# Kernel tuning notes

Hardware: AMD Instinct MI355X
Metric: run time of the kernel (lower is better)

Reference implementation:

```python
import jax, jax.numpy as jnp
import numpy as np

N, E, D = 50000, 600000, 128  # nodes, edges, units (== vert_dim, so no W_adapt)


def glorot(key, shape):
    lim = np.sqrt(6.0 / (shape[0] + shape[1]))
    return jax.random.uniform(key, shape, jnp.float32, -lim, lim)


def setup_inputs() -> dict:
    key = jax.random.key(0)
    ks = jax.random.split(key, 8)
    X = jax.random.normal(ks[0], (N, D), jnp.float32)
    ref_a = jax.random.randint(ks[1], (E,), 0, N, jnp.int32)
    ref_b = jax.random.randint(ks[2], (E,), 0, N, jnp.int32)
    # msg_net: two Dense(D) layers, inner_activation=None (linear)
    W1 = glorot(ks[3], (D, D)); b1 = jnp.zeros((D,), jnp.float32)
    W2 = glorot(ks[4], (D, D)); b2 = jnp.zeros((D,), jnp.float32)
    # keras GRUCell (reset_after=True): kernel [D,3D], recurrent_kernel [D,3D], bias [2,3D]
    gru_kernel = glorot(ks[5], (D, 3 * D))
    gru_rkernel = glorot(ks[6], (D, 3 * D))
    gru_bias = jnp.zeros((2, 3 * D), jnp.float32)
    return {"X": X, "ref_a": ref_a, "ref_b": ref_b,
            "W1": W1, "b1": b1, "W2": W2, "b2": b2,
            "gru_kernel": gru_kernel, "gru_rkernel": gru_rkernel, "gru_bias": gru_bias}


def _ggnn(X, ref_a, ref_b, W1, b1, W2, b2, gru_kernel, gru_rkernel, gru_bias):
    # msg_net (depth=2, linear inner activation)
    X_msg = (X @ W1 + b1) @ W2 + b2                       # [N, D]
    # wl1_convolution, undirected: scatter-add both directions
    agg = jnp.zeros_like(X_msg)
    agg = agg.at[ref_b].add(X_msg[ref_a])                 # a -> b
    agg = agg.at[ref_a].add(X_msg[ref_b])                 # b -> a (directed=False)
    # keras GRUCell update: inputs = agg, state = X  (reset_after=True)
    mx = agg @ gru_kernel + gru_bias[0]                   # [N, 3D]
    mh = X @ gru_rkernel + gru_bias[1]                    # [N, 3D]
    xz, xr, xh = jnp.split(mx, 3, axis=-1)
    rz, rr, rh = jnp.split(mh, 3, axis=-1)
    z = jax.nn.sigmoid(xz + rz)
    r = jax.nn.sigmoid(xr + rr)
    hh = jnp.tanh(xh + r * rh)
    return z * X + (1.0 - z) * hh                         # [N, D]


def reference(X, ref_a, ref_b, W1, b1, W2, b2, gru_kernel, gru_rkernel, gru_bias):
    return _ggnn(X, ref_a, ref_b, W1, b1, W2, b2, gru_kernel, gru_rkernel, gru_bias)
```

## Files before the change

kernel.cpp:

```cpp
#include <hip/hip_runtime.h>
#include <cstdint>
#include <cstddef>

typedef __bf16 bf16x8 __attribute__((ext_vector_type(8)));
typedef float  f32x4  __attribute__((ext_vector_type(4)));
typedef short  s16x8  __attribute__((ext_vector_type(8)));

static __device__ __forceinline__ float bf2f(short s) {
    union { unsigned u; float f; } v;
    v.u = ((unsigned)(unsigned short)s) << 16;
    return v.f;
}
static __device__ __forceinline__ short f2bf(float f) {
    unsigned u = __float_as_uint(f);
    u += 0x7fffu + ((u >> 16) & 1u);
    return (short)(u >> 16);
}
static __device__ __forceinline__ float rcp_(float x) {
    return __builtin_amdgcn_rcpf(x);
}
static __device__ __forceinline__ float sigmoid_(float x) {
    return rcp_(1.0f + __expf(-x));
}
static __device__ __forceinline__ float tanh_(float x) {
    float ax = fabsf(x);
    float e  = __expf(-2.0f * ax);
    float t  = (1.0f - e) * rcp_(1.0f + e);
    return copysignf(t, x);
}

#define MFMA(a, b, c) __builtin_amdgcn_mfma_f32_16x16x32_bf16((a), (b), (c), 0, 0, 0)

static __device__ __forceinline__ int lidx8(int r, int ch) {
    return r * 128 + ((ch ^ (r & 15)) << 3);
}
static __device__ __forceinline__ int lidx(int r, int col) {
    return r * 128 + ((((col >> 3) ^ (r & 15)) << 3) | (col & 7));
}

#define BLOCKS1     256
#define STRIPE_CAP  32
#define BUCKET_REG  (BLOCKS1 * STRIPE_CAP)
#define NODE_CAP    96

static __device__ __forceinline__ s16x8 cvt8(const float* p) {
    f32x4 a0 = *(const f32x4*)(p);
    f32x4 a1 = *(const f32x4*)(p + 4);
    s16x8 v;
    v[0] = f2bf(a0[0]); v[1] = f2bf(a0[1]); v[2] = f2bf(a0[2]); v[3] = f2bf(a0[3]);
    v[4] = f2bf(a1[0]); v[5] = f2bf(a1[1]); v[6] = f2bf(a1[2]); v[7] = f2bf(a1[3]);
    return v;
}

__global__ __launch_bounds__(512) void pass1_msg_kernel(
    const int* __restrict__ ra, const int* __restrict__ rb,
    unsigned* __restrict__ bucketed, int* __restrict__ stripeCnt,
    int E, int CPB, int nbk,
    const float* __restrict__ GK, const float* __restrict__ GR,
    short* __restrict__ GKt, short* __restrict__ GRt,
    const float* __restrict__ X,
    const float* __restrict__ W1, const float* __restrict__ b1,
    const float* __restrict__ W2, const float* __restrict__ b2,
    short* __restrict__ msg, int N)
{
    __shared__ short ldsA[64 * 128];
    __shared__ short ldsY[64 * 128];
    __shared__ int cnt[1024];
    const int tid = threadIdx.x;

    if ((int)blockIdx.x < BLOCKS1) {
        for (int b = tid; b < nbk; b += 512) cnt[b] = 0;

        int i = blockIdx.x * 512 + tid;
        if (i < 49152) {
            int k = i / 384, n = i - k * 384;
            GKt[n * 128 + k] = f2bf(GK[i]);
            GRt[n * 128 + k] = f2bf(GR[i]);
        }
        __syncthreads();

        const int blk = blockIdx.x;
        const int e1 = min(E, (blk + 1) * CPB);
        for (int e = blk * CPB + tid; e < e1; e += 512) {
            int a = ra[e], b = rb[e];
            int ka = a >> 6, kb = b >> 6;
            int r1 = atomicAdd(&cnt[ka], 1);
            if (r1 < STRIPE_CAP)
                bucketed[(size_t)ka * BUCKET_REG + blk * STRIPE_CAP + r1] =
                    ((unsigned)(a & 63) << 16) | (unsigned)b;
            int r2 = atomicAdd(&cnt[kb], 1);
            if (r2 < STRIPE_CAP)
                bucketed[(size_t)kb * BUCKET_REG + blk * STRIPE_CAP + r2] =
                    ((unsigned)(b & 63) << 16) | (unsigned)a;
        }
        __syncthreads();
        for (int b = tid; b < nbk; b += 512)
            stripeCnt[(size_t)b * BLOCKS1 + blk] = min(cnt[b], STRIPE_CAP);
        return;
    }

    const int m0   = (blockIdx.x - BLOCKS1) * 64;
    const int lane = tid & 63, wv = tid >> 6;
    const int q = lane >> 4, c = lane & 15;
    const int ncol = wv * 16 + c;

    bf16x8 w1f[4], w2f[4];
#pragma unroll
    for (int ks = 0; ks < 4; ks++) {
        s16x8 v1, v2;
#pragma unroll
        for (int t = 0; t < 8; t++) {
            int k = ks * 32 + q * 8 + t;
            v1[t] = f2bf(W1[(size_t)k * 128 + ncol]);
            v2[t] = f2bf(W2[(size_t)k * 128 + ncol]);
        }
        w1f[ks] = __builtin_bit_cast(bf16x8, v1);
        w2f[ks] = __builtin_bit_cast(bf16x8, v2);
    }

    for (int i = tid; i < 64 * 16; i += 512) {
        int r = i >> 4, ch = i & 15;
        s16x8 v;
        if (m0 + r < N) v = cvt8(X + (size_t)(m0 + r) * 128 + ch * 8);
        else            v = (s16x8)0;
        *(s16x8*)(ldsA + lidx8(r, ch)) = v;
    }
    __syncthreads();

    f32x4 acc[4];
#pragma unroll
    for (int rt = 0; rt < 4; rt++) acc[rt] = (f32x4)0.0f;
#pragma unroll
    for (int ks = 0; ks < 4; ks++) {
        int kc = ks * 4 + q;
#pragma unroll
        for (int rt = 0; rt < 4; rt++) {
            bf16x8 aA = __builtin_bit_cast(bf16x8, *(const s16x8*)(ldsA + lidx8(rt * 16 + c, kc)));
            acc[rt] = MFMA(aA, w1f[ks], acc[rt]);
        }
    }
    float bias1 = b1[ncol];
#pragma unroll
    for (int rt = 0; rt < 4; rt++)
#pragma unroll
        for (int i = 0; i < 4; i++)
            ldsY[lidx(rt * 16 + q * 4 + i, ncol)] = f2bf(acc[rt][i] + bias1);
    __syncthreads();

#pragma unroll
    for (int rt = 0; rt < 4; rt++) acc[rt] = (f32x4)0.0f;
#pragma unroll
    for (int ks = 0; ks < 4; ks++) {
        int kc = ks * 4 + q;
#pragma unroll
        for (int rt = 0; rt < 4; rt++) {
            bf16x8 aY = __builtin_bit_cast(bf16x8, *(const s16x8*)(ldsY + lidx8(rt * 16 + c, kc)));
            acc[rt] = MFMA(aY, w2f[ks], acc[rt]);
        }
    }
    float bias2 = b2[ncol];
#pragma unroll
    for (int rt = 0; rt < 4; rt++)
#pragma unroll
        for (int i = 0; i < 4; i++) {
            int row = m0 + rt * 16 + q * 4 + i;
            if (row < N) msg[(size_t)row * 128 + ncol] = f2bf(acc[rt][i] + bias2);
        }
}

__global__ __launch_bounds__(512) void slab_gather_kernel(
    const unsigned* __restrict__ bucketed, const int* __restrict__ stripeCnt,
    const short* __restrict__ msg, short* __restrict__ aggb, int N)
{
    __shared__ unsigned short slab[64 * NODE_CAP];
    __shared__ int off[64];
    __shared__ int scnt[BLOCKS1];
    const int tid = threadIdx.x;
    const int b   = blockIdx.x;

    if (tid < 64) off[tid] = 0;
    if (tid < BLOCKS1) scnt[tid] = stripeCnt[(size_t)b * BLOCKS1 + tid];
    __syncthreads();

    const unsigned* reg = bucketed + (size_t)b * BUCKET_REG;
    for (int i = tid; i < BUCKET_REG; i += 512) {
        if ((i & (STRIPE_CAP - 1)) < scnt[i >> 5]) {
            unsigned e = reg[i];
            int nl = (int)(e >> 16);
            int p  = (int)(e & 0xffffu);
            int r  = atomicAdd(&off[nl], 1);
            if (r < NODE_CAP)
                slab[nl * NODE_CAP + r] = (unsigned short)p;
        }
    }
    __syncthreads();

    const int lane = tid & 63, wv = tid >> 6;
    const int q  = lane >> 4;
    const int cl = lane & 15;

    for (int k = 0; k < 8; k++) {
        const int nl   = wv * 8 + k;
        const int node = b * 64 + nl;
        float a[8];
#pragma unroll
        for (int t = 0; t < 8; t++) a[t] = 0.0f;
        if (node < N) {
            const int deg = min(off[nl], NODE_CAP);
            const unsigned short* lst = slab + nl * NODE_CAP;
            int i = q;
            for (; i + 12 < deg; i += 16) {
                int j0 = (int)lst[i];
                int j1 = (int)lst[i + 4];
                int j2 = (int)lst[i + 8];
                int j3 = (int)lst[i + 12];
                s16x8 p0 = *(const s16x8*)(msg + (size_t)j0 * 128 + cl * 8);
                s16x8 p1 = *(const s16x8*)(msg + (size_t)j1 * 128 + cl * 8);
                s16x8 p2 = *(const s16x8*)(msg + (size_t)j2 * 128 + cl * 8);
                s16x8 p3 = *(const s16x8*)(msg + (size_t)j3 * 128 + cl * 8);
#pragma unroll
                for (int t = 0; t < 8; t++) a[t] += bf2f(p0[t]);
#pragma unroll
                for (int t = 0; t < 8; t++) a[t] += bf2f(p1[t]);
#pragma unroll
                for (int t = 0; t < 8; t++) a[t] += bf2f(p2[t]);
#pragma unroll
                for (int t = 0; t < 8; t++) a[t] += bf2f(p3[t]);
            }
            for (; i + 4 < deg; i += 8) {
                int j0 = (int)lst[i];
                int j1 = (int)lst[i + 4];
                s16x8 p0 = *(const s16x8*)(msg + (size_t)j0 * 128 + cl * 8);
                s16x8 p1 = *(const s16x8*)(msg + (size_t)j1 * 128 + cl * 8);
#pragma unroll
                for (int t = 0; t < 8; t++) a[t] += bf2f(p0[t]);
#pragma unroll
                for (int t = 0; t < 8; t++) a[t] += bf2f(p1[t]);
            }
            if (i < deg) {
                int j = (int)lst[i];
                s16x8 p = *(const s16x8*)(msg + (size_t)j * 128 + cl * 8);
#pragma unroll
                for (int t = 0; t < 8; t++) a[t] += bf2f(p[t]);
            }
        }
#pragma unroll
        for (int t = 0; t < 8; t++) {
            a[t] += __shfl_xor(a[t], 32);
            a[t] += __shfl_xor(a[t], 16);
        }
        if (q == 0 && b * 64 + nl < N) {
            s16x8 o;
#pragma unroll
            for (int t = 0; t < 8; t++) o[t] = f2bf(a[t]);
            *(s16x8*)(aggb + (size_t)(b * 64 + nl) * 128 + cl * 8) = o;
        }
    }
}

__global__ __launch_bounds__(512) void gru_kernel(
    const short* __restrict__ aggb, const float* __restrict__ X,
    const short* __restrict__ GKt, const short* __restrict__ GRt,
    const float* __restrict__ gbias, float* __restrict__ out, int N)
{
    __shared__ short ldsA[64 * 128];
    __shared__ short ldsX[64 * 128];
    const int tid  = threadIdx.x;
    const int m0   = blockIdx.x * 64;
    const int lane = tid & 63, wv = tid >> 6;
    const int q = lane >> 4, c = lane & 15;
    const int ncol = wv * 16 + c;

    bf16x8 bkz[4], bkr[4], bkh[4], brz[4], brr[4], brh[4];
#pragma unroll
    for (int ks = 0; ks < 4; ks++) {
        int ko = ks * 32 + q * 8;
        bkz[ks] = __builtin_bit_cast(bf16x8, *(const s16x8*)(GKt + (size_t)(ncol)       * 128 + ko));
        bkr[ks] = __builtin_bit_cast(bf16x8, *(const s16x8*)(GKt + (size_t)(128 + ncol) * 128 + ko));
        bkh[ks] = __builtin_bit_cast(bf16x8, *(const s16x8*)(GKt + (size_t)(256 + ncol) * 128 + ko));
        brz[ks] = __builtin_bit_cast(bf16x8, *(const s16x8*)(GRt + (size_t)(ncol)       * 128 + ko));
        brr[ks] = __builtin_bit_cast(bf16x8, *(const s16x8*)(GRt + (size_t)(128 + ncol) * 128 + ko));
        brh[ks] = __builtin_bit_cast(bf16x8, *(const s16x8*)(GRt + (size_t)(256 + ncol) * 128 + ko));
    }
    float bz0 = gbias[ncol],       br0 = gbias[128 + ncol],       bh0 = gbias[256 + ncol];
    float bz1 = gbias[384 + ncol], br1 = gbias[384 + 128 + ncol], bh1 = gbias[384 + 256 + ncol];

    for (int i = tid; i < 64 * 16; i += 512) {
        int r = i >> 4, ch = i & 15;
        s16x8 vx, va;
        if (m0 + r < N) {
            vx = cvt8(X + (size_t)(m0 + r) * 128 + ch * 8);
            va = *(const s16x8*)(aggb + (size_t)(m0 + r) * 128 + ch * 8);
        } else { vx = (s16x8)0; va = (s16x8)0; }
        *(s16x8*)(ldsX + lidx8(r, ch)) = vx;
        *(s16x8*)(ldsA + lidx8(r, ch)) = va;
    }
    __syncthreads();

#pragma clang loop unroll(disable)
    for (int rt = 0; rt < 4; rt++) {
        float xv[4];
#pragma unroll
        for (int i = 0; i < 4; i++) {
            int grow = m0 + rt * 16 + q * 4 + i;
            xv[i] = (grow < N) ? X[(size_t)grow * 128 + ncol] : 0.0f;
        }
        f32x4 axz = (f32x4)0.0f, axr = (f32x4)0.0f, axh = (f32x4)0.0f;
        f32x4 arz = (f32x4)0.0f, arr = (f32x4)0.0f, arh = (f32x4)0.0f;
#pragma unroll
        for (int ks = 0; ks < 4; ks++) {
            int kc = ks * 4 + q;
            bf16x8 aA = __builtin_bit_cast(bf16x8, *(const s16x8*)(ldsA + lidx8(rt * 16 + c, kc)));
            bf16x8 aX = __builtin_bit_cast(bf16x8, *(const s16x8*)(ldsX + lidx8(rt * 16 + c, kc)));
            axz = MFMA(aA, bkz[ks], axz);
            axr = MFMA(aA, bkr[ks], axr);
            axh = MFMA(aA, bkh[ks], axh);
            arz = MFMA(aX, brz[ks], arz);
            arr = MFMA(aX, brr[ks], arr);
            arh = MFMA(aX, brh[ks], arh);
        }
#pragma unroll
        for (int i = 0; i < 4; i++) {
            int grow = m0 + rt * 16 + q * 4 + i;
            if (grow < N) {
                float z  = sigmoid_(axz[i] + bz0 + arz[i] + bz1);
                float r  = sigmoid_(axr[i] + br0 + arr[i] + br1);
                float hh = tanh_(axh[i] + bh0 + r * (arh[i] + bh1));
                out[(size_t)grow * 128 + ncol] = z * xv[i] + (1.0f - z) * hh;
            }
        }
    }
}

extern "C" void kernel_launch(void* const* d_in, const int* in_sizes, int n_in,
                              void* d_out, int out_size, void* d_ws, size_t ws_size,
                              hipStream_t stream)
{
    const float* X  = (const float*)d_in[0];
    const int*   ra = (const int*)d_in[1];
    const int*   rb = (const int*)d_in[2];
    const float* W1 = (const float*)d_in[3];
    const float* b1 = (const float*)d_in[4];
    const float* W2 = (const float*)d_in[5];
    const float* b2 = (const float*)d_in[6];
    const float* GK = (const float*)d_in[7];
    const float* GR = (const float*)d_in[8];
    const float* GB = (const float*)d_in[9];
    const int N = in_sizes[0] / 128;
    const int E = in_sizes[1];
    float* out = (float*)d_out;

    const int nbk = (N + 63) / 64;

    char* ws = (char*)d_ws;
    size_t off = 0;
    short* aggb   = (short*)(ws + off);   off += (size_t)N * 128 * 2;
    short* msg    = (short*)(ws + off);   off += (size_t)N * 128 * 2;
    short* GKt    = (short*)(ws + off);   off += 49152u * 2;
    short* GRt    = (short*)(ws + off);   off += 49152u * 2;
    unsigned* bucketed = (unsigned*)(ws + off);
    off += (size_t)nbk * BUCKET_REG * 4;
    int* stripeCnt = (int*)(ws + off);    off += (size_t)nbk * BLOCKS1 * 4;

    const int CPB = (E + BLOCKS1 - 1) / BLOCKS1;

    pass1_msg_kernel<<<BLOCKS1 + nbk, 512, 0, stream>>>(
        ra, rb, bucketed, stripeCnt, E, CPB, nbk,
        GK, GR, GKt, GRt,
        X, W1, b1, W2, b2, msg, N);

    slab_gather_kernel<<<nbk, 512, 0, stream>>>(bucketed, stripeCnt, msg, aggb, N);

    gru_kernel<<<nbk, 512, 0, stream>>>(aggb, X, GKt, GRt, GB, out, N);
}
```

Measured before the change: 200.9 us.

## Fuse slab gather and GRU update into one tail kernel via LDS

Merges the neighbor-aggregation gather kernel with the GRU kernel so the aggregated bf16 rows are written straight into shared memory and consumed by the MFMA GRU step in the same block. This removes the global aggb round trip (write plus read of N×128 bf16) and one kernel launch. In exchange, per-block LDS usage grows (slab plus two 64×128 tiles) and register pressure combines both phases, with launch_bounds(512,6) hinting occupancy, which may lower concurrency for the latency-bound gather.

```diff
diff --git a/kernel.cpp b/kernel.cpp
--- a/kernel.cpp
+++ b/kernel.cpp
@@ -168,18 +168,31 @@
         }
 }
 
-__global__ __launch_bounds__(512) void slab_gather_kernel(
+__global__ __launch_bounds__(512, 6) void tail_kernel(
     const unsigned* __restrict__ bucketed, const int* __restrict__ stripeCnt,
-    const short* __restrict__ msg, short* __restrict__ aggb, int N)
+    const short* __restrict__ msg, const float* __restrict__ X,
+    const short* __restrict__ GKt, const short* __restrict__ GRt,
+    const float* __restrict__ gbias, float* __restrict__ out, int N)
 {
+    __shared__ short ldsA[64 * 128];
+    __shared__ short ldsX[64 * 128];
     __shared__ unsigned short slab[64 * NODE_CAP];
     __shared__ int off[64];
     __shared__ int scnt[BLOCKS1];
     const int tid = threadIdx.x;
     const int b   = blockIdx.x;
+    const int m0  = b * 64;
 
     if (tid < 64) off[tid] = 0;
     if (tid < BLOCKS1) scnt[tid] = stripeCnt[(size_t)b * BLOCKS1 + tid];
+
+    for (int i = tid; i < 64 * 16; i += 512) {
+        int r = i >> 4, ch = i & 15;
+        s16x8 vx;
+        if (m0 + r < N) vx = cvt8(X + (size_t)(m0 + r) * 128 + ch * 8);
+        else            vx = (s16x8)0;
+        *(s16x8*)(ldsX + lidx8(r, ch)) = vx;
+    }
     __syncthreads();
 
     const unsigned* reg = bucketed + (size_t)b * BUCKET_REG;
@@ -198,14 +211,14 @@
     const int lane = tid & 63, wv = tid >> 6;
     const int q  = lane >> 4;
     const int cl = lane & 15;
+    const int ncol = wv * 16 + cl;
 
     for (int k = 0; k < 8; k++) {
-        const int nl   = wv * 8 + k;
-        const int node = b * 64 + nl;
+        const int nl = wv * 8 + k;
         float a[8];
 #pragma unroll
         for (int t = 0; t < 8; t++) a[t] = 0.0f;
-        if (node < N) {
+        {
             const int deg = min(off[nl], NODE_CAP);
             const unsigned short* lst = slab + nl * NODE_CAP;
             int i = q;
@@ -249,27 +262,13 @@
             a[t] += __shfl_xor(a[t], 32);
             a[t] += __shfl_xor(a[t], 16);
         }
-        if (q == 0 && b * 64 + nl < N) {
+        if (q == 0) {
             s16x8 o;
 #pragma unroll
             for (int t = 0; t < 8; t++) o[t] = f2bf(a[t]);
-            *(s16x8*)(aggb + (size_t)(b * 64 + nl) * 128 + cl * 8) = o;
-        }
-    }
-}
-
-__global__ __launch_bounds__(512) void gru_kernel(
-    const short* __restrict__ aggb, const float* __restrict__ X,
-    const short* __restrict__ GKt, const short* __restrict__ GRt,
-    const float* __restrict__ gbias, float* __restrict__ out, int N)
-{
-    __shared__ short ldsA[64 * 128];
-    __shared__ short ldsX[64 * 128];
-    const int tid  = threadIdx.x;
-    const int m0   = blockIdx.x * 64;
-    const int lane = tid & 63, wv = tid >> 6;
-    const int q = lane >> 4, c = lane & 15;
-    const int ncol = wv * 16 + c;
+            *(s16x8*)(ldsA + lidx8(nl, cl)) = o;
+        }
+    }
 
     bf16x8 bkz[4], bkr[4], bkh[4], brz[4], brr[4], brh[4];
 #pragma unroll
@@ -284,17 +283,6 @@
     }
     float bz0 = gbias[ncol],       br0 = gbias[128 + ncol],       bh0 = gbias[256 + ncol];
     float bz1 = gbias[384 + ncol], br1 = gbias[384 + 128 + ncol], bh1 = gbias[384 + 256 + ncol];
-
-    for (int i = tid; i < 64 * 16; i += 512) {
-        int r = i >> 4, ch = i & 15;
-        s16x8 vx, va;
-        if (m0 + r < N) {
-            vx = cvt8(X + (size_t)(m0 + r) * 128 + ch * 8);
-            va = *(const s16x8*)(aggb + (size_t)(m0 + r) * 128 + ch * 8);
-        } else { vx = (s16x8)0; va = (s16x8)0; }
-        *(s16x8*)(ldsX + lidx8(r, ch)) = vx;
-        *(s16x8*)(ldsA + lidx8(r, ch)) = va;
-    }
     __syncthreads();
 
 #pragma clang loop unroll(disable)
@@ -310,8 +298,8 @@
 #pragma unroll
         for (int ks = 0; ks < 4; ks++) {
             int kc = ks * 4 + q;
-            bf16x8 aA = __builtin_bit_cast(bf16x8, *(const s16x8*)(ldsA + lidx8(rt * 16 + c, kc)));
-            bf16x8 aX = __builtin_bit_cast(bf16x8, *(const s16x8*)(ldsX + lidx8(rt * 16 + c, kc)));
+            bf16x8 aA = __builtin_bit_cast(bf16x8, *(const s16x8*)(ldsA + lidx8(rt * 16 + cl, kc)));
+            bf16x8 aX = __builtin_bit_cast(bf16x8, *(const s16x8*)(ldsX + lidx8(rt * 16 + cl, kc)));
             axz = MFMA(aA, bkz[ks], axz);
             axr = MFMA(aA, bkr[ks], axr);
             axh = MFMA(aA, bkh[ks], axh);
@@ -354,7 +342,6 @@
 
     char* ws = (char*)d_ws;
     size_t off = 0;
-    short* aggb   = (short*)(ws + off);   off += (size_t)N * 128 * 2;
     short* msg    = (short*)(ws + off);   off += (size_t)N * 128 * 2;
     short* GKt    = (short*)(ws + off);   off += 49152u * 2;
     short* GRt    = (short*)(ws + off);   off += 49152u * 2;
@@ -369,7 +356,6 @@
         GK, GR, GKt, GRt,
         X, W1, b1, W2, b2, msg, N);
 
-    slab_gather_kernel<<<nbk, 512, 0, stream>>>(bucketed, stripeCnt, msg, aggb, N);
-
-    gru_kernel<<<nbk, 512, 0, stream>>>(aggb, X, GKt, GRt, GB, out, N);
-}
+    tail_kernel<<<nbk, 512, 0, stream>>>(
+        bucketed, stripeCnt, msg, X, GKt, GRt, GB, out, N);
+}
```

Measured after the change: 292.2 us. 1.45x slower.

## Coarsen edge buckets to 256 nodes and split each bucket over four gather blocks

Applied to the files above, without the earlier changes.

Edge bucketing in pass1 now groups edges by 256-node ranges instead of 64-node ranges, with wider per-stripe capacity. This cuts the number of bucket counters and the number of scattered bucket regions written. Each gather block now scans a whole 256-node bucket and keeps only the entries for its own 64-node quarter. The cost is that every bucket is read four times, and the stripe capacity per source block must still be enough to avoid dropping edges.

```diff
diff --git a/kernel.cpp b/kernel.cpp
--- a/kernel.cpp
+++ b/kernel.cpp
@@ -39,7 +39,7 @@
 }
 
 #define BLOCKS1     256
-#define STRIPE_CAP  32
+#define STRIPE_CAP  64
 #define BUCKET_REG  (BLOCKS1 * STRIPE_CAP)
 #define NODE_CAP    96
 
@@ -55,7 +55,7 @@
 __global__ __launch_bounds__(512) void pass1_msg_kernel(
     const int* __restrict__ ra, const int* __restrict__ rb,
     unsigned* __restrict__ bucketed, int* __restrict__ stripeCnt,
-    int E, int CPB, int nbk,
+    int E, int CPB, int nbuckets,
     const float* __restrict__ GK, const float* __restrict__ GR,
     short* __restrict__ GKt, short* __restrict__ GRt,
     const float* __restrict__ X,
@@ -65,11 +65,11 @@
 {
     __shared__ short ldsA[64 * 128];
     __shared__ short ldsY[64 * 128];
-    __shared__ int cnt[1024];
+    __shared__ int cnt[256];
     const int tid = threadIdx.x;
 
     if ((int)blockIdx.x < BLOCKS1) {
-        for (int b = tid; b < nbk; b += 512) cnt[b] = 0;
+        if (tid < 256) cnt[tid] = 0;
 
         int i = blockIdx.x * 512 + tid;
         if (i < 49152) {
@@ -83,19 +83,19 @@
         const int e1 = min(E, (blk + 1) * CPB);
         for (int e = blk * CPB + tid; e < e1; e += 512) {
             int a = ra[e], b = rb[e];
-            int ka = a >> 6, kb = b >> 6;
+            int ka = a >> 8, kb = b >> 8;
             int r1 = atomicAdd(&cnt[ka], 1);
             if (r1 < STRIPE_CAP)
                 bucketed[(size_t)ka * BUCKET_REG + blk * STRIPE_CAP + r1] =
-                    ((unsigned)(a & 63) << 16) | (unsigned)b;
+                    ((unsigned)(a & 255) << 16) | (unsigned)b;
             int r2 = atomicAdd(&cnt[kb], 1);
             if (r2 < STRIPE_CAP)
                 bucketed[(size_t)kb * BUCKET_REG + blk * STRIPE_CAP + r2] =
-                    ((unsigned)(b & 63) << 16) | (unsigned)a;
+                    ((unsigned)(b & 255) << 16) | (unsigned)a;
         }
         __syncthreads();
-        for (int b = tid; b < nbk; b += 512)
-            stripeCnt[(size_t)b * BLOCKS1 + blk] = min(cnt[b], STRIPE_CAP);
+        if (tid < nbuckets)
+            stripeCnt[(size_t)tid * BLOCKS1 + blk] = min(cnt[tid], STRIPE_CAP);
         return;
     }
 
@@ -176,21 +176,25 @@
     __shared__ int off[64];
     __shared__ int scnt[BLOCKS1];
     const int tid = threadIdx.x;
-    const int b   = blockIdx.x;
+    const int t   = blockIdx.x;
+    const int k   = t >> 2;
+    const int qt  = t & 3;
 
     if (tid < 64) off[tid] = 0;
-    if (tid < BLOCKS1) scnt[tid] = stripeCnt[(size_t)b * BLOCKS1 + tid];
-    __syncthreads();
-
-    const unsigned* reg = bucketed + (size_t)b * BUCKET_REG;
+    if (tid < BLOCKS1) scnt[tid] = stripeCnt[(size_t)k * BLOCKS1 + tid];
+    __syncthreads();
+
+    const unsigned* reg = bucketed + (size_t)k * BUCKET_REG;
     for (int i = tid; i < BUCKET_REG; i += 512) {
-        if ((i & (STRIPE_CAP - 1)) < scnt[i >> 5]) {
+        if ((i & (STRIPE_CAP - 1)) < scnt[i >> 6]) {
             unsigned e = reg[i];
             int nl = (int)(e >> 16);
-            int p  = (int)(e & 0xffffu);
-            int r  = atomicAdd(&off[nl], 1);
-            if (r < NODE_CAP)
-                slab[nl * NODE_CAP + r] = (unsigned short)p;
+            if ((nl >> 6) == qt) {
+                int p = (int)(e & 0xffffu);
+                int r = atomicAdd(&off[nl & 63], 1);
+                if (r < NODE_CAP)
+                    slab[(nl & 63) * NODE_CAP + r] = (unsigned short)p;
+            }
         }
     }
     __syncthreads();
@@ -199,12 +203,12 @@
     const int q  = lane >> 4;
     const int cl = lane & 15;
 
-    for (int k = 0; k < 8; k++) {
-        const int nl   = wv * 8 + k;
-        const int node = b * 64 + nl;
+    for (int kk = 0; kk < 8; kk++) {
+        const int nl   = wv * 8 + kk;
+        const int node = t * 64 + nl;
         float a[8];
 #pragma unroll
-        for (int t = 0; t < 8; t++) a[t] = 0.0f;
+        for (int tt = 0; tt < 8; tt++) a[tt] = 0.0f;
         if (node < N) {
             const int deg = min(off[nl], NODE_CAP);
             const unsigned short* lst = slab + nl * NODE_CAP;
@@ -219,13 +223,13 @@
                 s16x8 p2 = *(const s16x8*)(msg + (size_t)j2 * 128 + cl * 8);
                 s16x8 p3 = *(const s16x8*)(msg + (size_t)j3 * 128 + cl * 8);
 #pragma unroll
-                for (int t = 0; t < 8; t++) a[t] += bf2f(p0[t]);
-#pragma unroll
-                for (int t = 0; t < 8; t++) a[t] += bf2f(p1[t]);
-#pragma unroll
-                for (int t = 0; t < 8; t++) a[t] += bf2f(p2[t]);
-#pragma unroll
-                for (int t = 0; t < 8; t++) a[t] += bf2f(p3[t]);
+                for (int tt = 0; tt < 8; tt++) a[tt] += bf2f(p0[tt]);
+#pragma unroll
+                for (int tt = 0; tt < 8; tt++) a[tt] += bf2f(p1[tt]);
+#pragma unroll
+                for (int tt = 0; tt < 8; tt++) a[tt] += bf2f(p2[tt]);
+#pragma unroll
+                for (int tt = 0; tt < 8; tt++) a[tt] += bf2f(p3[tt]);
             }
             for (; i + 4 < deg; i += 8) {
                 int j0 = (int)lst[i];
@@ -233,27 +237,27 @@
                 s16x8 p0 = *(const s16x8*)(msg + (size_t)j0 * 128 + cl * 8);
                 s16x8 p1 = *(const s16x8*)(msg + (size_t)j1 * 128 + cl * 8);
 #pragma unroll
-                for (int t = 0; t < 8; t++) a[t] += bf2f(p0[t]);
-#pragma unroll
-                for (int t = 0; t < 8; t++) a[t] += bf2f(p1[t]);
+                for (int tt = 0; tt < 8; tt++) a[tt] += bf2f(p0[tt]);
+#pragma unroll
+                for (int tt = 0; tt < 8; tt++) a[tt] += bf2f(p1[tt]);
             }
             if (i < deg) {
                 int j = (int)lst[i];
                 s16x8 p = *(const s16x8*)(msg + (size_t)j * 128 + cl * 8);
 #pragma unroll
-                for (int t = 0; t < 8; t++) a[t] += bf2f(p[t]);
-            }
-        }
-#pragma unroll
-        for (int t = 0; t < 8; t++) {
-            a[t] += __shfl_xor(a[t], 32);
-            a[t] += __shfl_xor(a[t], 16);
-        }
-        if (q == 0 && b * 64 + nl < N) {
+                for (int tt = 0; tt < 8; tt++) a[tt] += bf2f(p[tt]);
+            }
+        }
+#pragma unroll
+        for (int tt = 0; tt < 8; tt++) {
+            a[tt] += __shfl_xor(a[tt], 32);
+            a[tt] += __shfl_xor(a[tt], 16);
+        }
+        if (q == 0 && node < N) {
             s16x8 o;
 #pragma unroll
-            for (int t = 0; t < 8; t++) o[t] = f2bf(a[t]);
-            *(s16x8*)(aggb + (size_t)(b * 64 + nl) * 128 + cl * 8) = o;
+            for (int tt = 0; tt < 8; tt++) o[tt] = f2bf(a[tt]);
+            *(s16x8*)(aggb + (size_t)node * 128 + cl * 8) = o;
         }
     }
 }
@@ -350,7 +354,8 @@
     const int E = in_sizes[1];
     float* out = (float*)d_out;
 
-    const int nbk = (N + 63) / 64;
+    const int nbuckets = (N + 255) >> 8;
+    const int nblk64   = (N + 63) / 64;
 
     char* ws = (char*)d_ws;
     size_t off = 0;
@@ -359,17 +364,18 @@
     short* GKt    = (short*)(ws + off);   off += 49152u * 2;
     short* GRt    = (short*)(ws + off);   off += 49152u * 2;
     unsigned* bucketed = (unsigned*)(ws + off);
-    off += (size_t)nbk * BUCKET_REG * 4;
-    int* stripeCnt = (int*)(ws + off);    off += (size_t)nbk * BLOCKS1 * 4;
+    off += (size_t)nbuckets * BUCKET_REG * 4;
+    int* stripeCnt = (int*)(ws + off);    off += (size_t)nbuckets * BLOCKS1 * 4;
 
     const int CPB = (E + BLOCKS1 - 1) / BLOCKS1;
 
-    pass1_msg_kernel<<<BLOCKS1 + nbk, 512, 0, stream>>>(
-        ra, rb, bucketed, stripeCnt, E, CPB, nbk,
+    pass1_msg_kernel<<<BLOCKS1 + nblk64, 512, 0, stream>>>(
+        ra, rb, bucketed, stripeCnt, E, CPB, nbuckets,
         GK, GR, GKt, GRt,
         X, W1, b1, W2, b2, msg, N);
 
-    slab_gather_kernel<<<nbk, 512, 0, stream>>>(bucketed, stripeCnt, msg, aggb, N);
-
-    gru_kernel<<<nbk, 512, 0, stream>>>(aggb, X, GKt, GRt, GB, out, N);
-}
+    slab_gather_kernel<<<nblk64, 512, 0, stream>>>(
+        bucketed, stripeCnt, msg, aggb, N);
+
+    gru_kernel<<<nblk64, 512, 0, stream>>>(aggb, X, GKt, GRt, GB, out, N);
+}
```

Measured after the change: 203.8 us. Within noise of the previous version (+1.4%).
